# Kernel optimization log

Measured on AMD Instinct MI355X. Metric: run time of the kernel, lower is better.

The kernel has to match this reference:

```python
import jax, jax.numpy as jnp
import numpy as np

C = 8; E = 512; HEADS = 8; DH = E // HEADS; M = 256; PINV_ITERS = 6; KW = 33

def layer_norm(x, g, b):
    mu = x.mean(-1, keepdims=True)
    xm = x - mu
    v = (xm * xm).mean(-1, keepdims=True)
    return xm / jnp.sqrt(v + 1e-5) * g + b

def mp_pinv(x, iters=PINV_ITERS):
    # Moore-Penrose pseudoinverse via Newton-Schulz iterations (lucidrains nystrom-attention)
    I = jnp.eye(x.shape[-1], dtype=x.dtype)
    ax = jnp.abs(x)
    z = jnp.swapaxes(x, -1, -2) / (jnp.max(ax.sum(-2)) * jnp.max(ax.sum(-1)))
    for _ in range(iters):
        xz = x @ z
        z = 0.25 * z @ (13. * I - xz @ (15. * I - xz @ (7. * I - xz)))
    return z

def nystrom_attn(x, mask, Wqkv, Wout, bout, conv_w):
    b, n0, d = x.shape
    pad = (-n0) % M  # left-pad so seq divisible by num_landmarks
    x = jnp.pad(x, ((0, 0), (pad, 0), (0, 0)))
    mask = jnp.pad(mask, ((0, 0), (pad, 0)))
    n = n0 + pad
    qkv = (x @ Wqkv).reshape(b, n, 3, HEADS, DH).transpose(2, 0, 3, 1, 4)
    q, k, v = qkv[0], qkv[1], qkv[2]  # [b,h,n,dh]
    mf = mask[:, None, :, None].astype(x.dtype)
    q = q * mf * (DH ** -0.5); k = k * mf; v = v * mf
    l = n // M
    mls = mask.reshape(b, 1, M, l).sum(-1).astype(x.dtype)  # valid count per landmark segment
    div = mls[..., None] + 1e-8
    ql = q.reshape(b, HEADS, M, l, DH).sum(3) / div
    kl = k.reshape(b, HEADS, M, l, DH).sum(3) / div
    mland = mls > 0  # [b,1,M]
    neg = -jnp.finfo(x.dtype).max / 2
    sim1 = jnp.where(mask[:, None, :, None] & mland[..., None, :], jnp.einsum('bhid,bhjd->bhij', q, kl), neg)
    sim2 = jnp.where(mland[..., :, None] & mland[..., None, :], jnp.einsum('bhid,bhjd->bhij', ql, kl), neg)
    sim3 = jnp.where(mland[..., :, None] & mask[:, None, None, :], jnp.einsum('bhid,bhjd->bhij', ql, k), neg)
    a1 = jax.nn.softmax(sim1, -1); a2 = jax.nn.softmax(sim2, -1); a3 = jax.nn.softmax(sim3, -1)
    out = (a1 @ mp_pinv(a2)) @ (a3 @ v)
    # residual depthwise conv over sequence dim (residual=True in NystromAttention)
    out = out + jax.lax.conv_general_dilated(v, conv_w, (1, 1), ((KW // 2, KW // 2), (0, 0)),
                                             dimension_numbers=('NCHW', 'OIHW', 'NCHW'),
                                             feature_group_count=HEADS)
    out = out.transpose(0, 2, 1, 3).reshape(b, n, d) @ Wout + bout
    return out[:, pad:]

def _forward(h, W1, b1, cls_token, pmt_token, ln1_g, ln1_b, Wqkv1, Wout1, bout1, conv1,
             ln0_g, ln0_b, Wqkv0, Wout0, bout0, conv0, lnf_g, lnf_b, W3, b3):
    N = h.shape[0]
    h1 = jax.nn.relu(h @ W1 + b1)  # _fc1
    seq = jnp.concatenate([cls_token, pmt_token, h1], 0)[None]  # [1, 1+C+N, E]
    y = nystrom_attn(layer_norm(seq, ln1_g, ln1_b), jnp.ones((1, seq.shape[1]), bool),
                     Wqkv1, Wout1, bout1, conv1)
    x = seq + y  # layer1 (TransLayer_custom)
    pmt = x[:, 1:1 + C, :]   # new pmt tokens [1,C,E]
    toks = x[:, 1 + C:, :]   # [1,N,E]
    assn = jax.nn.softmax(jnp.einsum('bnd,bcd->bnc', toks, pmt), -1)
    idx = jnp.argmax(assn[0], -1)  # [N] cluster assignment
    # cluster dispatch: per-cluster [pmt_i; tokens-of-cluster-i] run of shared layer0, via masking
    xs = jnp.concatenate([pmt[0][:, None, :], jnp.broadcast_to(toks[0], (C, N, E))], 1)  # [C,1+N,E]
    masks = jnp.concatenate([jnp.ones((C, 1), bool), idx[None, :] == jnp.arange(C)[:, None]], 1)
    def trans0(xi, mi):
        xi = xi[None]
        return (xi + nystrom_attn(layer_norm(xi, ln0_g, ln0_b), mi[None], Wqkv0, Wout0, bout0, conv0))[0]
    out = jax.vmap(trans0)(xs, masks)  # [C,1+N,E]
    h_un = out[:, 1:, :][idx, jnp.arange(N)]  # each token from its own cluster's run
    order = jnp.argsort(idx)  # stable: groups tokens by cluster, preserving order (concat order)
    h_global = h_un[order]; idx_new = idx[order]
    hcat = jnp.concatenate([x[0, 0][None], h_global], 0)  # [1+N, E]
    hn = layer_norm(hcat, lnf_g, lnf_b)
    sums = jax.ops.segment_sum(hcat[1:], idx_new, num_segments=C)
    counts = jax.ops.segment_sum(jnp.ones((N,), h.dtype), idx_new, num_segments=C)
    merge = sums / jnp.maximum(counts, 1.)[:, None]  # CTM merge token per cluster
    ptc = jnp.linalg.norm(pmt[0] @ pmt[0].T - jnp.eye(C, dtype=h.dtype))
    tok_out = jnp.concatenate([hn[0][None], merge], 0).mean(0)
    logit = tok_out @ W3 + b3
    return logit, ptc

def setup_inputs() -> dict:
    key = jax.random.key(0)
    ks = jax.random.split(key, 16)
    N, IN_DIM, NC = 4096, 1024, 2
    s = 0.02
    q, _ = jnp.linalg.qr(jax.random.normal(ks[15], (E, C)))  # orthonormal pmt init
    return {
        'h': jax.random.normal(ks[0], (N, IN_DIM)),
        'W1': jax.random.normal(ks[1], (IN_DIM, E)) * s, 'b1': jnp.zeros((E,)),
        'cls_token': jax.random.normal(ks[2], (1, E)),
        'pmt_token': q.T,
        'ln1_g': jnp.ones((E,)), 'ln1_b': jnp.zeros((E,)),
        'Wqkv1': jax.random.normal(ks[3], (E, 3 * E)) * s,
        'Wout1': jax.random.normal(ks[4], (E, E)) * s, 'bout1': jnp.zeros((E,)),
        'conv1': jax.random.normal(ks[5], (HEADS, 1, KW, 1)) * s,
        'ln0_g': jnp.ones((E,)), 'ln0_b': jnp.zeros((E,)),
        'Wqkv0': jax.random.normal(ks[6], (E, 3 * E)) * s,
        'Wout0': jax.random.normal(ks[7], (E, E)) * s, 'bout0': jnp.zeros((E,)),
        'conv0': jax.random.normal(ks[8], (HEADS, 1, KW, 1)) * s,
        'lnf_g': jnp.ones((E,)), 'lnf_b': jnp.zeros((E,)),
        'W3': jax.random.normal(ks[9], (E, NC)) * s, 'b3': jnp.zeros((NC,)),
    }

def reference(h, W1, b1, cls_token, pmt_token, ln1_g, ln1_b, Wqkv1, Wout1, bout1, conv1,
              ln0_g, ln0_b, Wqkv0, Wout0, bout0, conv0, lnf_g, lnf_b, W3, b3):
    logit, ptc = _forward(h, W1, b1, cls_token, pmt_token, ln1_g, ln1_b, Wqkv1, Wout1, bout1, conv1,
                          ln0_g, ln0_b, Wqkv0, Wout0, bout0, conv0, lnf_g, lnf_b, W3, b3)
    return (logit[None], jax.nn.softmax(logit)[None], ptc)
```

## Files before the change

kernel.cpp:

```cpp
#include <hip/hip_runtime.h>

#define NEGV (-1.70141173e38f)

constexpr int E    = 512;
constexpr int NTOK = 4096;
constexpr int NPAD = 4352;
constexpr int PAD1 = 247;
constexpr int NSEQ = 4105;
constexpr int NG   = 5120;
constexpr int NTP  = 4104;

typedef __attribute__((ext_vector_type(8))) short short8;
typedef __attribute__((ext_vector_type(4))) float float4v;

__device__ inline float bf2f(ushort u){ return __uint_as_float(((unsigned)u)<<16); }
__device__ inline ushort f2bf(float f){
  unsigned u = __float_as_uint(f);
  unsigned r = (u + 0x7FFFu + ((u>>16)&1u)) >> 16;
  return (ushort)r;
}

template<int BT, bool BOUNDS>
__global__ __launch_bounds__(256) void k_mm(
    const ushort* __restrict__ A, const ushort* __restrict__ B,
    const float* __restrict__ bias, const float* __restrict__ resid,
    float* __restrict__ Cf, ushort* __restrict__ Cb,
    int M, int N, int K, int ksplit, int ldC,
    long sA, long sB, long sC,
    const int* __restrict__ colsel, const int* __restrict__ rowsel,
    int zmodA, int zmodB, const int* __restrict__ krange, int kshift,
    float alpha, float bdiag, int flags)
{
  const int z = blockIdx.z;
  const int batch = z / ksplit, ks = z - batch * ksplit;
  const int kslice = K / ksplit;
  int kbeg = ks * kslice, kend = kbeg + kslice;
  if (krange) { int ki = batch >> kshift; kbeg = krange[2*ki]; kend = krange[2*ki+1]; }
  long aoff;
  if (colsel) { int s = colsel[blockIdx.x]; if (s < 0) s = 0; aoff = (long)(s*8 + batch) * sA; }
  else aoff = (long)(zmodA ? (batch & (zmodA-1)) : batch) * sA;
  long boff;
  if (rowsel) { int s = rowsel[blockIdx.y]; if (s < 0) s = 0; boff = (long)(s*8 + batch) * sB; }
  else boff = (long)(zmodB ? (batch & (zmodB-1)) : batch) * sB;
  A += aoff; B += boff;
  const long coff = (long)z * sC;

  __shared__ __align__(16) ushort Al[4][128][8];
  __shared__ __align__(16) ushort Bl[4][128][8];

  const int tid  = threadIdx.x;
  const int lane = tid & 63, wid = tid >> 6;
  const int wr = wid >> 1, wc = wid & 1;
  const int l4 = lane >> 4, l15 = lane & 15;
  const int row0 = blockIdx.y * 128, col0 = blockIdx.x * 128;

  float4v acc[4][4];
#pragma unroll
  for (int i = 0; i < 4; ++i)
#pragma unroll
    for (int j = 0; j < 4; ++j) acc[i][j] = (float4v){0.f,0.f,0.f,0.f};

  for (int k0 = kbeg; k0 < kend; k0 += 32) {
    __syncthreads();
#pragma unroll
    for (int e = 0; e < 2; ++e) {
      int id = tid * 2 + e; int m = id >> 2, kb = id & 3;
      uint4 v = make_uint4(0u,0u,0u,0u);
      int gr = row0 + m;
      if (!BOUNDS || gr < M)
        v = *reinterpret_cast<const uint4*>(A + (long)gr * K + k0 + kb * 8);
      *reinterpret_cast<uint4*>(&Al[kb][m][0]) = v;
    }
    if (BT) {
#pragma unroll
      for (int e = 0; e < 2; ++e) {
        int id = tid * 2 + e; int n = id >> 2, kb = id & 3;
        uint4 v = make_uint4(0u,0u,0u,0u);
        int gc = col0 + n;
        if (!BOUNDS || gc < N)
          v = *reinterpret_cast<const uint4*>(B + (long)gc * K + k0 + kb * 8);
        *reinterpret_cast<uint4*>(&Bl[kb][n][0]) = v;
      }
    } else {
      int n = tid & 127, gc = col0 + n;
      bool inb = (!BOUNDS || gc < N);
#pragma unroll
      for (int e = 0; e < 2; ++e) {
        int kb = (tid >> 7) * 2 + e;
        ushort u[8];
#pragma unroll
        for (int j = 0; j < 8; ++j) {
          int gk = k0 + kb * 8 + j;
          ushort val = inb ? B[(long)gk * N + gc] : (ushort)0;
          if (flags & 4) {
            float f = bdiag * (gk == gc ? 1.f : 0.f) - bf2f(val);
            val = f2bf(f);
          }
          u[j] = val;
        }
        uint4 w;
        w.x = (unsigned)u[0] | ((unsigned)u[1] << 16);
        w.y = (unsigned)u[2] | ((unsigned)u[3] << 16);
        w.z = (unsigned)u[4] | ((unsigned)u[5] << 16);
        w.w = (unsigned)u[6] | ((unsigned)u[7] << 16);
        *reinterpret_cast<uint4*>(&Bl[kb][n][0]) = w;
      }
    }
    __syncthreads();
    short8 af[4], bg[4];
#pragma unroll
    for (int mi = 0; mi < 4; ++mi)
      af[mi] = *reinterpret_cast<const short8*>(&Al[l4][wr*64 + mi*16 + l15][0]);
#pragma unroll
    for (int ni = 0; ni < 4; ++ni)
      bg[ni] = *reinterpret_cast<const short8*>(&Bl[l4][wc*64 + ni*16 + l15][0]);
#pragma unroll
    for (int mi = 0; mi < 4; ++mi)
#pragma unroll
      for (int ni = 0; ni < 4; ++ni)
        acc[mi][ni] = __builtin_amdgcn_mfma_f32_16x16x32_bf16(af[mi], bg[ni], acc[mi][ni], 0, 0, 0);
  }
#pragma unroll
  for (int mi = 0; mi < 4; ++mi)
#pragma unroll
    for (int ni = 0; ni < 4; ++ni)
#pragma unroll
      for (int r = 0; r < 4; ++r) {
        int row = row0 + wr*64 + mi*16 + l4*4 + r;
        int col = col0 + wc*64 + ni*16 + l15;
        if (BOUNDS && (row >= M || col >= N)) continue;
        float v = alpha * acc[mi][ni][r];
        if (flags & 1) v += bias[col];
        if (flags & 2) v = fmaxf(v, 0.f);
        if (flags & 8) v += resid[(long)row * ldC + col];
        long off = coff + (long)row * ldC + col;
        if (flags & 16) Cb[off] = f2bf(v); else Cf[off] = v;
      }
}

static void mm(hipStream_t st, const void* A, const void* B, const float* bias, const float* resid,
               float* Cf, ushort* Cb, int M, int N, int K, int nb, int ksplit, int ldC,
               long sA, long sB, long sC,
               const int* colsel, const int* rowsel, int zmodA, int zmodB,
               const int* krange, int kshift,
               float alpha, float bdiag, int flags, bool bt, bool bounds)
{
  dim3 g((N + 127) / 128, (M + 127) / 128, nb * ksplit), b(256);
  const ushort* a = (const ushort*)A; const ushort* bb = (const ushort*)B;
  if (bt) {
    if (bounds) k_mm<1, true ><<<g, b, 0, st>>>(a, bb, bias, resid, Cf, Cb, M, N, K, ksplit, ldC, sA, sB, sC, colsel, rowsel, zmodA, zmodB, krange, kshift, alpha, bdiag, flags);
    else        k_mm<1, false><<<g, b, 0, st>>>(a, bb, bias, resid, Cf, Cb, M, N, K, ksplit, ldC, sA, sB, sC, colsel, rowsel, zmodA, zmodB, krange, kshift, alpha, bdiag, flags);
  } else {
    if (bounds) k_mm<0, true ><<<g, b, 0, st>>>(a, bb, bias, resid, Cf, Cb, M, N, K, ksplit, ldC, sA, sB, sC, colsel, rowsel, zmodA, zmodB, krange, kshift, alpha, bdiag, flags);
    else        k_mm<0, false><<<g, b, 0, st>>>(a, bb, bias, resid, Cf, Cb, M, N, K, ksplit, ldC, sA, sB, sC, colsel, rowsel, zmodA, zmodB, krange, kshift, alpha, bdiag, flags);
  }
}

static void pinv_iters(hipStream_t st, const ushort* PX, ushort* PZ, ushort* Y, ushort* T1, ushort* T2, int nb) {
  ushort* z = PZ; ushort* y = Y;
  for (int it = 0; it < 6; ++it) {
    mm(st, PX, z,  nullptr, nullptr, nullptr, y,  256,256,256, nb,1,256, 65536,65536,65536, nullptr,nullptr,0,0,nullptr,0, 1.f,   0.f, 16,    false, false);
    mm(st, y,  y,  nullptr, nullptr, nullptr, T1, 256,256,256, nb,1,256, 65536,65536,65536, nullptr,nullptr,0,0,nullptr,0, 1.f,   7.f, 16|4,  false, false);
    mm(st, y,  T1, nullptr, nullptr, nullptr, T2, 256,256,256, nb,1,256, 65536,65536,65536, nullptr,nullptr,0,0,nullptr,0, 1.f,  15.f, 16|4,  false, false);
    mm(st, z,  T2, nullptr, nullptr, nullptr, y,  256,256,256, nb,1,256, 65536,65536,65536, nullptr,nullptr,0,0,nullptr,0, 0.25f,13.f, 16|4,  false, false);
    ushort* tmp = z; z = y; y = tmp;
  }
}

__global__ void k_z0(const ushort* __restrict__ X, const float* __restrict__ sc, ushort* __restrict__ Z, int nb) {
  long t = (long)blockIdx.x * 256 + threadIdx.x;
  if (t >= (long)nb * 65536) return;
  int bt = (int)(t >> 16); int ij = (int)(t & 65535); int i = ij >> 8, j = ij & 255;
  Z[t] = f2bf(bf2f(X[((long)bt << 16) + j * 256 + i]) * sc[bt >> 3]);
}

__global__ __launch_bounds__(256) void k_colmax(const ushort* __restrict__ X, float* __restrict__ sc) {
  int cl = blockIdx.x, j = threadIdx.x;
  float cmax = 0.f;
  for (int h = 0; h < 8; ++h) {
    const ushort* mat = X + (long)(cl * 8 + h) * 65536;
    float cs = 0.f;
    for (int i = 0; i < 256; ++i) cs += bf2f(mat[i * 256 + j]);
    cmax = fmaxf(cmax, cs);
  }
  __shared__ float red[256];
  red[j] = cmax; __syncthreads();
  for (int o = 128; o > 0; o >>= 1) { if (j < o) red[j] = fmaxf(red[j], red[j + o]); __syncthreads(); }
  if (j == 0) sc[cl] = 1.f / red[0];
}

__global__ void k_prep0(const float* __restrict__ cls, const float* __restrict__ pmt, float* __restrict__ seq) {
  int i = blockIdx.x * 256 + threadIdx.x;
  if (i < 512) seq[i] = cls[i];
  else if (i < 4608) seq[i] = pmt[i - 512];
}
__global__ void k_cvt(const float* __restrict__ s, ushort* __restrict__ d, long n) {
  long i = (long)blockIdx.x * 256 + threadIdx.x;
  if (i < n) d[i] = f2bf(s[i]);
}
__global__ void k_tcvt_all(const float* __restrict__ W1, const float* __restrict__ Wq1,
                           const float* __restrict__ Wq0, const float* __restrict__ Wo1,
                           const float* __restrict__ Wo0,
                           ushort* __restrict__ W1t, ushort* __restrict__ Wq1t,
                           ushort* __restrict__ Wq0t, ushort* __restrict__ Wo1t,
                           ushort* __restrict__ Wo0t) {
  const float* W; ushort* Wt; int K, N;
  switch (blockIdx.z) {
    case 0:  W = W1;  Wt = W1t;  K = 1024; N = 512;  break;
    case 1:  W = Wq1; Wt = Wq1t; K = 512;  N = 1536; break;
    case 2:  W = Wq0; Wt = Wq0t; K = 512;  N = 1536; break;
    case 3:  W = Wo1; Wt = Wo1t; K = 512;  N = 512;  break;
    default: W = Wo0; Wt = Wo0t; K = 512;  N = 512;  break;
  }
  int nb_ = blockIdx.x * 32, kb = blockIdx.y * 32;
  if (nb_ >= N || kb >= K) return;
  __shared__ float tile[32][33];
  int tx = threadIdx.x, ty = threadIdx.y;
  for (int r = ty; r < 32; r += 8) tile[r][tx] = W[(long)(kb + r) * N + nb_ + tx];
  __syncthreads();
  for (int r = ty; r < 32; r += 8) Wt[(long)(nb_ + r) * K + kb + tx] = f2bf(tile[tx][r]);
}

__device__ __forceinline__ void ln_row(const float* __restrict__ xr, const float* __restrict__ g,
                                       const float* __restrict__ b, ushort* __restrict__ yr,
                                       float* red, int t) {
  float v0 = xr[t], v1 = xr[t + 256];
  red[t] = v0 + v1; __syncthreads();
  for (int o = 128; o > 0; o >>= 1) { if (t < o) red[t] += red[t + o]; __syncthreads(); }
  float mu = red[0] * (1.f / E); __syncthreads();
  float d0 = v0 - mu, d1 = v1 - mu;
  red[t] = d0 * d0 + d1 * d1; __syncthreads();
  for (int o = 128; o > 0; o >>= 1) { if (t < o) red[t] += red[t + o]; __syncthreads(); }
  float inv = 1.f / sqrtf(red[0] * (1.f / E) + 1e-5f);
  yr[t]       = f2bf(d0 * inv * g[t]       + b[t]);
  yr[t + 256] = f2bf(d1 * inv * g[t + 256] + b[t + 256]);
}

__global__ __launch_bounds__(256) void k_lnB(const float* __restrict__ x, const float* __restrict__ g,
                                             const float* __restrict__ b, ushort* __restrict__ y) {
  int row = blockIdx.x, t = threadIdx.x;
  ushort* yr = y + (long)row * E;
  if (row < PAD1) { yr[t] = 0; yr[t + 256] = 0; return; }
  __shared__ float red[256];
  ln_row(x + (long)(row - PAD1) * E, g, b, yr, red, t);
}
__global__ __launch_bounds__(256) void k_lnC(const float* __restrict__ seq, const float* __restrict__ g,
                                             const float* __restrict__ b, ushort* __restrict__ y) {
  int row = blockIdx.x, t = threadIdx.x;
  const float* xr = (row < 8) ? (seq + 512 + (long)row * E) : (seq + 9 * 512 + (long)(row - 8) * E);
  __shared__ float red[256];
  ln_row(xr, g, b, y + (long)row * E, red, t);
}

__global__ void k_buildQKVB(const float* __restrict__ qkv, ushort* __restrict__ Qb,
                            ushort* __restrict__ Kb, ushort* __restrict__ Vt) {
  int h = blockIdx.y, p0 = blockIdx.x * 64;
  int tx = threadIdx.x & 63, tg = threadIdx.x >> 6;
  __shared__ float tile[64][65];
  for (int r = tg; r < 64; r += 4) {
    long src = (long)(p0 + r) * 1536 + h * 64 + tx;
    long o = ((long)h * NPAD + p0 + r) * 64 + tx;
    Qb[o] = f2bf(qkv[src]);
    Kb[o] = f2bf(qkv[src + 512]);
    tile[r][tx] = qkv[src + 1024];
  }
  __syncthreads();
  for (int d = tg; d < 64; d += 4) Vt[((long)h * 64 + d) * NPAD + p0 + tx] = f2bf(tile[tx][d]);
}
__global__ void k_gatherQKV(const float* __restrict__ qkvall, const int* __restrict__ gtok,
                            ushort* __restrict__ Qg, ushort* __restrict__ Kg, ushort* __restrict__ Vgt) {
  int h = blockIdx.y, p0 = blockIdx.x * 64;
  int tx = threadIdx.x & 63, tg = threadIdx.x >> 6;
  __shared__ float tile[64][65];
  for (int r = tg; r < 64; r += 4) {
    int tk = gtok[p0 + r];
    int srcrow = tk >= 0 ? 8 + tk : (tk <= -2 ? (-2 - tk) : -1);
    float q = 0.f, k = 0.f, v = 0.f;
    if (srcrow >= 0) {
      long s = (long)srcrow * 1536 + h * 64 + tx;
      q = qkvall[s]; k = qkvall[s + 512]; v = qkvall[s + 1024];
    }
    long o = ((long)h * NG + p0 + r) * 64 + tx;
    Qg[o] = f2bf(q); Kg[o] = f2bf(k);
    tile[r][tx] = v;
  }
  __syncthreads();
  for (int d = tg; d < 64; d += 4) Vgt[((long)h * 64 + d) * NG + p0 + tx] = f2bf(tile[tx][d]);
}

__global__ void k_qlkl_B(const float* __restrict__ qkv, ushort* __restrict__ ql, ushort* __restrict__ kl,
                         float* __restrict__ mlandB) {
  int i = blockIdx.x, h = blockIdx.y, d = threadIdx.x;
  float sq = 0.f, sk = 0.f; int cnt = 0;
  for (int j = 0; j < 17; ++j) {
    int p = i * 17 + j;
    if (p >= PAD1) {
      sq += qkv[(long)p * 1536 + h * 64 + d];
      sk += qkv[(long)p * 1536 + 512 + h * 64 + d];
      cnt++;
    }
  }
  float dv = (float)cnt + 1e-8f;
  ql[((long)h * 256 + i) * 64 + d] = f2bf(sq * 0.125f / dv);
  kl[((long)h * 256 + i) * 64 + d] = f2bf(sk / dv);
  if (h == 0 && d == 0) mlandB[i] = cnt > 0 ? 1.f : 0.f;
}

__global__ void k_qlkl_C(const float* __restrict__ qkvall, const int* __restrict__ idx,
                         ushort* __restrict__ qlc, ushort* __restrict__ klc,
                         float* __restrict__ mland_c) {
  int i = blockIdx.x, bt = blockIdx.y;
  int c = bt >> 3, h = bt & 7, d = threadIdx.x;
  float sq = 0.f, sk = 0.f; int cnt = 0;
  for (int j = 0; j < 17; ++j) {
    int p = i * 17 + j;
    int srcrow = -1;
    if (p == 255) srcrow = c;
    else if (p >= 256 && idx[p - 256] == c) srcrow = 8 + (p - 256);
    if (srcrow >= 0) {
      const float* src = qkvall + (long)srcrow * 1536 + h * 64;
      sq += src[d]; sk += src[512 + d];
      cnt++;
    }
  }
  float dv = (float)cnt + 1e-8f;
  qlc[((long)bt * 256 + i) * 64 + d] = f2bf(sq * 0.125f / dv);
  klc[((long)bt * 256 + i) * 64 + d] = f2bf(sk / dv);
  if (h == 0 && d == 0) mland_c[c * 256 + i] = cnt > 0 ? 1.f : 0.f;
}

__global__ __launch_bounds__(256) void k_a2soft(const float* __restrict__ S2, const float* __restrict__ mland,
                                                ushort* __restrict__ X) {
  int i = blockIdx.x, bt = blockIdx.y, j = threadIdx.x;
  int cl = bt >> 3;
  const float* Sr = S2 + ((long)bt * 256 + i) * 256;
  __shared__ float red[256];
  float landi = mland[cl * 256 + i];
  float out;
  if (landi > 0.f) {
    bool valid = mland[cl * 256 + j] > 0.f;
    float sv = valid ? Sr[j] : NEGV;
    red[j] = sv; __syncthreads();
    for (int o = 128; o > 0; o >>= 1) { if (j < o) red[j] = fmaxf(red[j], red[j + o]); __syncthreads(); }
    float mx = red[0]; __syncthreads();
    float e = valid ? expf(sv - mx) : 0.f;
    red[j] = e; __syncthreads();
    for (int o = 128; o > 0; o >>= 1) { if (j < o) red[j] += red[j + o]; __syncthreads(); }
    out = e / red[0];
  } else {
    out = 1.f / 256.f;
  }
  X[((long)bt * 256 + i) * 256 + j] = f2bf(out);
}

__global__ __launch_bounds__(256) void k_smaxB_av(const float* __restrict__ S, ushort* __restrict__ P,
                                                  const float* __restrict__ mland) {
  int i = blockIdx.x, h = blockIdx.y, t = threadIdx.x;
  const float* Sr = S + ((long)h * 256 + i) * NPAD;
  ushort* Pr = P + ((long)h * 256 + i) * NPAD;
  __shared__ float sv[NPAD];
  __shared__ float red[256];
  if (mland[i] > 0.f) {
    float lmax = NEGV;
    for (int j = t; j < NPAD; j += 256) {
      float s = Sr[j];
      sv[j] = s;
      if (j >= PAD1) lmax = fmaxf(lmax, s);
    }
    red[t] = lmax; __syncthreads();
    for (int o = 128; o > 0; o >>= 1) { if (t < o) red[t] = fmaxf(red[t], red[t + o]); __syncthreads(); }
    float mx = red[0]; __syncthreads();
    float lsum = 0.f;
    for (int j = t; j < NPAD; j += 256) {
      float e = (j >= PAD1) ? expf(sv[j] - mx) : 0.f;
      sv[j] = e; lsum += e;
    }
    red[t] = lsum; __syncthreads();
    for (int o = 128; o > 0; o >>= 1) { if (t < o) red[t] += red[t + o]; __syncthreads(); }
    float inv = 1.f / red[0];
    for (int j = t; j < NPAD; j += 256) Pr[j] = f2bf(sv[j] * inv);
  } else {
    const float u = 1.f / 4352.f;
    for (int j = t; j < NPAD; j += 256) Pr[j] = f2bf(j >= PAD1 ? u : 0.f);
  }
}

__global__ __launch_bounds__(256) void k_smaxseg(const float* __restrict__ S3, ushort* __restrict__ P3,
                                                 const float* __restrict__ mlandC, const int* __restrict__ gclu,
                                                 const int* __restrict__ segb) {
  int i = blockIdx.x, bt = blockIdx.y, t = threadIdx.x;
  int c = bt >> 3, h = bt & 7;
  const float* Sr = S3 + ((long)h * 256 + i) * NG;
  ushort* Pr = P3 + ((long)h * 256 + i) * NG;
  int jb = segb[c], je = segb[c + 1];
  __shared__ float sv[4352];
  __shared__ float red[256];
  if (mlandC[c * 256 + i] > 0.f) {
    float lmax = NEGV;
    for (int j = jb + t; j < je; j += 256) {
      float s = Sr[j];
      sv[j - jb] = s;
      if (gclu[j] == c) lmax = fmaxf(lmax, s);
    }
    red[t] = lmax; __syncthreads();
    for (int o = 128; o > 0; o >>= 1) { if (t < o) red[t] = fmaxf(red[t], red[t + o]); __syncthreads(); }
    float mx = red[0]; __syncthreads();
    float lsum = 0.f;
    for (int j = jb + t; j < je; j += 256) {
      float e = (gclu[j] == c) ? expf(sv[j - jb] - mx) : 0.f;
      sv[j - jb] = e; lsum += e;
    }
    red[t] = lsum; __syncthreads();
    for (int o = 128; o > 0; o >>= 1) { if (t < o) red[t] += red[t + o]; __syncthreads(); }
    float inv = 1.f / red[0];
    for (int j = jb + t; j < je; j += 256) Pr[j] = f2bf(sv[j - jb] * inv);
  } else {
    const float u = 1.f / 4352.f;
    for (int j = jb + t; j < je; j += 256) Pr[j] = f2bf(gclu[j] == c ? u : 0.f);
  }
}

template<int MODE>
__global__ __launch_bounds__(256) void k_smax256(const float* __restrict__ S, ushort* __restrict__ P,
                                                 const float* __restrict__ mland, const int* __restrict__ gtok,
                                                 const int* __restrict__ gclu, int rows) {
  int row = blockIdx.x, h = blockIdx.y, j = threadIdx.x;
  const float* Sr = S + ((long)h * rows + row) * 256;
  ushort* Pr = P + ((long)h * rows + row) * 256;
  int c = 0;
  if (MODE == 1) {
    int tk = gtok[row];
    if (tk < 0) { Pr[j] = 0; return; }
    c = gclu[row];
  }
  bool mem = (MODE == 1) ? (mland[c * 256 + j] > 0.f) : (mland[j] > 0.f);
  __shared__ float red[256];
  float s = mem ? Sr[j] : NEGV;
  red[j] = s; __syncthreads();
  for (int o = 128; o > 0; o >>= 1) { if (j < o) red[j] = fmaxf(red[j], red[j + o]); __syncthreads(); }
  float mx = red[0]; __syncthreads();
  float e = mem ? expf(s - mx) : 0.f;
  red[j] = e; __syncthreads();
  for (int o = 128; o > 0; o >>= 1) { if (j < o) red[j] += red[j + o]; __syncthreads(); }
  Pr[j] = f2bf(e / red[0]);
}

__global__ void k_avredB(const float* __restrict__ sl, ushort* __restrict__ avb, int ks) {
  int i = blockIdx.x, h = blockIdx.y, d = threadIdx.x;
  float s = 0.f;
  for (int k = 0; k < ks; ++k) s += sl[(((long)h * ks + k) * 256 + i) * 64 + d];
  avb[((long)h * 256 + i) * 64 + d] = f2bf(s);
}

__global__ void k_conv_B(const float* __restrict__ qkv, const float* __restrict__ w,
                         const float* __restrict__ preout, ushort* __restrict__ lnb) {
  int r = blockIdx.x, t = threadIdx.x;
  int h = t >> 6;
  int prow = PAD1 + r;
  float acc = preout[(long)prow * E + t];
  for (int tt = 0; tt < 33; ++tt) {
    int p = prow + tt - 16;
    if (p < NPAD) acc += qkv[(long)p * 1536 + 1024 + t] * w[h * 33 + tt];
  }
  lnb[(long)r * E + t] = f2bf(acc);
}

__global__ void k_idxptc(const float* __restrict__ x, int* __restrict__ idx, float* __restrict__ ptc_out) {
  int t = threadIdx.x;
  __shared__ float red[64];
  if (blockIdx.x == NTOK) {
    int a = t >> 3, b = t & 7;
    const float* pmt = x + E;
    float s = 0.f;
    for (int d = 0; d < E; ++d) s += pmt[(long)a * E + d] * pmt[(long)b * E + d];
    s -= (a == b) ? 1.f : 0.f;
    red[t] = s * s; __syncthreads();
    for (int o = 32; o > 0; o >>= 1) { if (t < o) red[t] += red[t + o]; __syncthreads(); }
    if (t == 0) *ptc_out = sqrtf(red[0]);
    return;
  }
  int n = blockIdx.x;
  const float* tok = x + (long)(9 + n) * E;
  const float* pmt = x + E;
  int c = t >> 3, part = t & 7;
  float s = 0.f;
  for (int d = part * 64; d < part * 64 + 64; ++d) s += tok[d] * pmt[(long)c * E + d];
  red[t] = s; __syncthreads();
  if (t < 8) {
    float dot = 0.f;
    for (int p = 0; p < 8; ++p) dot += red[t * 8 + p];
    red[t] = dot;
  }
  __syncthreads();
  if (t == 0) {
    int best = 0; float bv = red[0];
    for (int c2 = 1; c2 < 8; ++c2) if (red[c2] > bv) { bv = red[c2]; best = c2; }
    idx[n] = best;
  }
}

__global__ __launch_bounds__(256) void k_gprep(const int* __restrict__ idx, int* __restrict__ gtok,
                                               int* __restrict__ gclu, int* __restrict__ gpos,
                                               int* __restrict__ segb, int* __restrict__ krange,
                                               int* __restrict__ blkclu) {
  __shared__ int hist[8][16];
  __shared__ int boff[8][16];
  __shared__ int segs[9];
  __shared__ int sidx[256];
  int t = threadIdx.x;
  if (t < 128) ((int*)hist)[t] = 0;
  __syncthreads();
  for (int b = 0; b < 16; ++b) atomicAdd(&hist[idx[b * 256 + t]][b], 1);
  __syncthreads();
  if (t == 0) {
    int s = 0;
    for (int c = 0; c < 8; ++c) {
      segs[c] = s;
      int run = s + 1, tot = 1;
      for (int b = 0; b < 16; ++b) { boff[c][b] = run; run += hist[c][b]; tot += hist[c][b]; }
      krange[2 * c] = s;
      krange[2 * c + 1] = s + ((tot + 31) & ~31);
      s += (tot + 127) & ~127;
    }
    segs[8] = s;
    for (int c = 0; c <= 8; ++c) segb[c] = segs[c];
  }
  __syncthreads();
  for (int g = t; g < NG; g += 256) { gtok[g] = -1; gclu[g] = -1; }
  __syncthreads();
  if (t < 8) { gtok[segs[t]] = -2 - t; gclu[segs[t]] = t; }
  for (int b = t; b < NG / 128; b += 256) {
    int cl = -1;
    for (int c = 0; c < 8; ++c) if (b * 128 >= segs[c] && b * 128 < segs[c + 1]) cl = c;
    blkclu[b] = cl;
  }
  for (int b = 0; b < 16; ++b) {
    int n = b * 256 + t;
    int c = idx[n];
    sidx[t] = c;
    __syncthreads();
    int rank = 0;
    for (int m = 0; m < t; ++m) rank += (sidx[m] == c);
    int pos = boff[c][b] + rank;
    gtok[pos] = n; gclu[pos] = c; gpos[n] = pos;
    __syncthreads();
  }
}

__global__ void k_outC(const float* __restrict__ OUTg, const int* __restrict__ gpos,
                       const int* __restrict__ idx, const float* __restrict__ qkvall,
                       const float* __restrict__ w, ushort* __restrict__ lnb) {
  int n = blockIdx.x, t = threadIdx.x;
  int h = t >> 6;
  int c = idx[n];
  float acc = OUTg[(long)gpos[n] * 512 + t];
  for (int tt = 0; tt < 33; ++tt) {
    int m = n + tt - 16;
    float vv = 0.f;
    if (m == -1) vv = qkvall[(long)c * 1536 + 1024 + t];
    else if (m >= 0 && m < NTOK && idx[m] == c) vv = qkvall[(long)(8 + m) * 1536 + 1024 + t];
    acc += vv * w[h * 33 + tt];
  }
  lnb[(long)n * E + t] = f2bf(acc);
}

__global__ void k_seg_part(const float* __restrict__ hun, const int* __restrict__ idx,
                           float* __restrict__ part, float* __restrict__ pcnt) {
  int c = blockIdx.x, sl = blockIdx.y, d = threadIdx.x;
  float s = 0.f; int cnt = 0;
  for (int n = sl * 256; n < sl * 256 + 256; ++n) {
    if (idx[n] == c) { s += hun[(long)n * E + d]; if (d == 0) cnt++; }
  }
  part[(long)(c * 16 + sl) * E + d] = s;
  if (d == 0) pcnt[c * 16 + sl] = (float)cnt;
}

__global__ void k_final(const float* __restrict__ x0, const float* __restrict__ g, const float* __restrict__ b,
                        const float* __restrict__ part, const float* __restrict__ pcnt,
                        const float* __restrict__ ptc, const float* __restrict__ W3, const float* __restrict__ b3,
                        float* __restrict__ out) {
  int t = threadIdx.x;
  __shared__ float red[512];
  float xv = x0[t];
  red[t] = xv; __syncthreads();
  for (int o = 256; o > 0; o >>= 1) { if (t < o) red[t] += red[t + o]; __syncthreads(); }
  float mu = red[0] * (1.f / 512.f); __syncthreads();
  float d0 = xv - mu;
  red[t] = d0 * d0; __syncthreads();
  for (int o = 256; o > 0; o >>= 1) { if (t < o) red[t] += red[t + o]; __syncthreads(); }
  float inv = 1.f / sqrtf(red[0] * (1.f / 512.f) + 1e-5f);
  __syncthreads();
  float acc = d0 * inv * g[t] + b[t];
  for (int c = 0; c < 8; ++c) {
    float s = 0.f, cnt = 0.f;
    for (int sl = 0; sl < 16; ++sl) { s += part[(long)(c * 16 + sl) * E + t]; cnt += pcnt[c * 16 + sl]; }
    acc += s / fmaxf(cnt, 1.f);
  }
  float tk = acc * (1.f / 9.f);
  red[t] = tk * W3[t * 2 + 0]; __syncthreads();
  for (int o = 256; o > 0; o >>= 1) { if (t < o) red[t] += red[t + o]; __syncthreads(); }
  float l0 = red[0] + b3[0]; __syncthreads();
  red[t] = tk * W3[t * 2 + 1]; __syncthreads();
  for (int o = 256; o > 0; o >>= 1) { if (t < o) red[t] += red[t + o]; __syncthreads(); }
  float l1 = red[0] + b3[1];
  if (t == 0) {
    out[0] = l0; out[1] = l1;
    float mx = fmaxf(l0, l1);
    float e0 = expf(l0 - mx), e1 = expf(l1 - mx), s = e0 + e1;
    out[2] = e0 / s; out[3] = e1 / s;
    out[4] = *ptc;
  }
}

extern "C" void kernel_launch(void* const* d_in, const int* in_sizes, int n_in,
                              void* d_out, int out_size, void* d_ws, size_t ws_size,
                              hipStream_t stream) {
  const float* h_in  = (const float*)d_in[0];
  const float* W1    = (const float*)d_in[1];
  const float* b1    = (const float*)d_in[2];
  const float* cls   = (const float*)d_in[3];
  const float* pmt_t = (const float*)d_in[4];
  const float* ln1_g = (const float*)d_in[5];
  const float* ln1_b = (const float*)d_in[6];
  const float* Wqkv1 = (const float*)d_in[7];
  const float* Wout1 = (const float*)d_in[8];
  const float* bout1 = (const float*)d_in[9];
  const float* conv1 = (const float*)d_in[10];
  const float* ln0_g = (const float*)d_in[11];
  const float* ln0_b = (const float*)d_in[12];
  const float* Wqkv0 = (const float*)d_in[13];
  const float* Wout0 = (const float*)d_in[14];
  const float* bout0 = (const float*)d_in[15];
  const float* conv0 = (const float*)d_in[16];
  const float* lnf_g = (const float*)d_in[17];
  const float* lnf_b = (const float*)d_in[18];
  const float* W3    = (const float*)d_in[19];
  const float* b3    = (const float*)d_in[20];

  char* base = (char*)d_ws;
  size_t off = 0;
  auto alloc = [&](size_t b) -> void* {
    off = (off + 255) & ~(size_t)255;
    void* p = base + off; off += b; return p;
  };
  float*  SEQ    = (float*) alloc((size_t)NSEQ * E * 4);
  float*  QKV    = (float*) alloc((size_t)NPAD * 1536 * 4);
  ushort* W1t    = (ushort*)alloc((size_t)512 * 1024 * 2);
  ushort* Wq1t   = (ushort*)alloc((size_t)1536 * 512 * 2);
  ushort* Wq0t   = (ushort*)alloc((size_t)1536 * 512 * 2);
  ushort* Wo1t   = (ushort*)alloc((size_t)512 * 512 * 2);
  ushort* Wo0t   = (ushort*)alloc((size_t)512 * 512 * 2);
  ushort* LNb    = (ushort*)alloc((size_t)NPAD * E * 2);
  ushort* QbU    = (ushort*)alloc((size_t)8 * NG * 64 * 2);
  ushort* KbU    = (ushort*)alloc((size_t)8 * NG * 64 * 2);
  ushort* VtU    = (ushort*)alloc((size_t)8 * NG * 64 * 2);
  char*   U1     = (char*)  alloc((size_t)8 * 256 * NG * 4);
  char*   U2     = (char*)  alloc((size_t)8 * 256 * NG * 2);
  ushort* PXb    = (ushort*)alloc((size_t)64 * 65536 * 2);
  ushort* PZa    = (ushort*)alloc((size_t)64 * 65536 * 2);
  ushort* qlbB   = (ushort*)alloc((size_t)8 * 16384 * 2);
  ushort* klbB   = (ushort*)alloc((size_t)8 * 16384 * 2);
  ushort* qlcb   = (ushort*)alloc((size_t)64 * 16384 * 2);
  ushort* klcb   = (ushort*)alloc((size_t)64 * 16384 * 2);
  float*  avsl   = (float*) alloc((size_t)8 * 8 * 16384 * 4);
  ushort* avb    = (ushort*)alloc((size_t)64 * 16384 * 2);
  ushort* Wcb    = (ushort*)alloc((size_t)64 * 16384 * 2);
  float*  PREOUT = (float*) alloc((size_t)NPAD * E * 4);
  float*  mlandB = (float*) alloc(256 * 4);
  float*  mlandC = (float*) alloc(8 * 256 * 4);
  int*    idx    = (int*)   alloc(NTOK * 4);
  int*    gtok   = (int*)   alloc(NG * 4);
  int*    gclu   = (int*)   alloc(NG * 4);
  int*    gpos   = (int*)   alloc(NTOK * 4);
  int*    segb   = (int*)   alloc(9 * 4);
  int*    krange = (int*)   alloc(16 * 4);
  int*    blkclu = (int*)   alloc((NG / 128) * 4);
  float*  ptc    = (float*) alloc(256);
  float*  sc     = (float*) alloc(256);
  float*  part   = (float*) alloc((size_t)8 * 16 * 512 * 4);
  float*  pcnt   = (float*) alloc(8 * 16 * 4);

  ushort* hb   = (ushort*)U1;
  float*  Sbuf = (float*)U1;
  ushort* Ybuf = (ushort*)U1;
  ushort* T1c  = (ushort*)(U1 + (size_t)64 * 65536 * 2);
  ushort* T2c  = (ushort*)(U1 + (size_t)2 * 64 * 65536 * 2);
  float*  OUTg = (float*)U1;
  ushort* Pbuf = (ushort*)U2;

  k_tcvt_all<<<dim3(48, 32, 5), dim3(32, 8), 0, stream>>>(W1, Wqkv1, Wqkv0, Wout1, Wout0,
                                                          W1t, Wq1t, Wq0t, Wo1t, Wo0t);
  k_prep0<<<dim3(18), dim3(256), 0, stream>>>(cls, pmt_t, SEQ);
  k_cvt<<<dim3(16384), dim3(256), 0, stream>>>(h_in, hb, (long)4096 * 1024);
  mm(stream, hb, W1t, b1, nullptr, SEQ + 9 * 512, nullptr, 4096, 512, 1024, 1, 1, 512,
     0, 0, 0, nullptr, nullptr, 0, 0, nullptr, 0, 1.f, 0.f, 1 | 2, true, false);

  k_lnB<<<dim3(NPAD), dim3(256), 0, stream>>>(SEQ, ln1_g, ln1_b, LNb);
  mm(stream, LNb, Wq1t, nullptr, nullptr, QKV, nullptr, NPAD, 1536, 512, 1, 1, 1536,
     0, 0, 0, nullptr, nullptr, 0, 0, nullptr, 0, 1.f, 0.f, 0, true, false);
  k_buildQKVB<<<dim3(NPAD / 64, 8), dim3(256), 0, stream>>>(QKV, QbU, KbU, VtU);
  k_qlkl_B<<<dim3(256, 8), dim3(64), 0, stream>>>(QKV, qlbB, klbB, mlandB);
  mm(stream, qlbB, klbB, nullptr, nullptr, Sbuf, nullptr, 256, 256, 64, 8, 1, 256,
     16384, 16384, 65536, nullptr, nullptr, 0, 0, nullptr, 0, 1.f, 0.f, 0, true, false);
  k_a2soft<<<dim3(256, 8), dim3(256), 0, stream>>>(Sbuf, mlandB, PXb);
  k_colmax<<<dim3(1), dim3(256), 0, stream>>>(PXb, sc);
  k_z0<<<dim3((8 * 65536) / 256), dim3(256), 0, stream>>>(PXb, sc, PZa, 8);
  pinv_iters(stream, PXb, PZa, Ybuf, T1c, T2c, 8);
  mm(stream, qlbB, KbU, nullptr, nullptr, Sbuf, nullptr, 256, NPAD, 64, 8, 1, NPAD,
     16384, (long)NPAD * 64, (long)256 * NPAD, nullptr, nullptr, 0, 0, nullptr, 0, 1.f, 0.f, 0, true, false);
  k_smaxB_av<<<dim3(256, 8), dim3(256), 0, stream>>>(Sbuf, Pbuf, mlandB);
  mm(stream, Pbuf, VtU, nullptr, nullptr, avsl, nullptr, 256, 64, NPAD, 8, 8, 64,
     (long)256 * NPAD, (long)64 * NPAD, 16384, nullptr, nullptr, 0, 0, nullptr, 0, 1.f, 0.f, 0, true, true);
  k_avredB<<<dim3(256, 8), dim3(64), 0, stream>>>(avsl, avb, 8);
  mm(stream, PZa, avb, nullptr, nullptr, nullptr, Wcb, 256, 64, 256, 8, 1, 64,
     65536, 16384, 16384, nullptr, nullptr, 0, 0, nullptr, 0, 1.f, 0.f, 16, false, true);
  mm(stream, QbU + PAD1 * 64, klbB, nullptr, nullptr, Sbuf, nullptr, NSEQ, 256, 64, 8, 1, 256,
     (long)NPAD * 64, 16384, (long)NSEQ * 256, nullptr, nullptr, 0, 0, nullptr, 0, 0.125f, 0.f, 0, true, true);
  k_smax256<0><<<dim3(NSEQ, 8), dim3(256), 0, stream>>>(Sbuf, Pbuf, mlandB, nullptr, nullptr, NSEQ);
  mm(stream, Pbuf, Wcb, nullptr, nullptr, PREOUT + (long)PAD1 * 512, nullptr, NSEQ, 64, 256, 8, 1, 512,
     (long)NSEQ * 256, 16384, 64, nullptr, nullptr, 0, 0, nullptr, 0, 1.f, 0.f, 0, false, true);
  k_conv_B<<<dim3(NSEQ), dim3(512), 0, stream>>>(QKV, conv1, PREOUT, LNb);
  mm(stream, LNb, Wo1t, bout1, SEQ, SEQ, nullptr, NSEQ, 512, 512, 1, 1, 512,
     0, 0, 0, nullptr, nullptr, 0, 0, nullptr, 0, 1.f, 0.f, 1 | 8, true, true);

  k_idxptc<<<dim3(NTOK + 1), dim3(64), 0, stream>>>(SEQ, idx, ptc);
  k_gprep<<<dim3(1), dim3(256), 0, stream>>>(idx, gtok, gclu, gpos, segb, krange, blkclu);
  k_lnC<<<dim3(NTP), dim3(256), 0, stream>>>(SEQ, ln0_g, ln0_b, LNb);
  mm(stream, LNb, Wq0t, nullptr, nullptr, QKV, nullptr, NTP, 1536, 512, 1, 1, 1536,
     0, 0, 0, nullptr, nullptr, 0, 0, nullptr, 0, 1.f, 0.f, 0, true, true);
  k_qlkl_C<<<dim3(256, 64), dim3(64), 0, stream>>>(QKV, idx, qlcb, klcb, mlandC);
  k_gatherQKV<<<dim3(NG / 64, 8), dim3(256), 0, stream>>>(QKV, gtok, QbU, KbU, VtU);
  mm(stream, qlcb, klcb, nullptr, nullptr, Sbuf, nullptr, 256, 256, 64, 64, 1, 256,
     16384, 16384, 65536, nullptr, nullptr, 0, 0, nullptr, 0, 1.f, 0.f, 0, true, false);
  k_a2soft<<<dim3(256, 64), dim3(256), 0, stream>>>(Sbuf, mlandC, PXb);
  k_colmax<<<dim3(8), dim3(256), 0, stream>>>(PXb, sc);
  k_z0<<<dim3((64 * 65536) / 256), dim3(256), 0, stream>>>(PXb, sc, PZa, 64);
  pinv_iters(stream, PXb, PZa, Ybuf, T1c, T2c, 64);
  mm(stream, qlcb, KbU, nullptr, nullptr, Sbuf, nullptr, 256, NG, 64, 8, 1, NG,
     16384, (long)NG * 64, (long)256 * NG, blkclu, nullptr, 0, 0, nullptr, 0, 1.f, 0.f, 0, true, false);
  k_smaxseg<<<dim3(256, 64), dim3(256), 0, stream>>>(Sbuf, Pbuf, mlandC, gclu, segb);
  mm(stream, Pbuf, VtU, nullptr, nullptr, nullptr, avb, 256, 64, NG, 64, 1, 64,
     (long)256 * NG, (long)64 * NG, 16384, nullptr, nullptr, 8, 8, krange, 3, 1.f, 0.f, 16, true, true);
  mm(stream, PZa, avb, nullptr, nullptr, nullptr, Wcb, 256, 64, 256, 64, 1, 64,
     65536, 16384, 16384, nullptr, nullptr, 0, 0, nullptr, 0, 1.f, 0.f, 16, false, true);
  mm(stream, QbU, klcb, nullptr, nullptr, Sbuf, nullptr, NG, 256, 64, 8, 1, 256,
     (long)NG * 64, 16384, (long)NG * 256, nullptr, blkclu, 0, 0, nullptr, 0, 0.125f, 0.f, 0, true, false);
  k_smax256<1><<<dim3(NG, 8), dim3(256), 0, stream>>>(Sbuf, Pbuf, mlandC, gtok, gclu, NG);
  mm(stream, Pbuf, Wcb, nullptr, nullptr, OUTg, nullptr, NG, 64, 256, 8, 1, 512,
     (long)NG * 256, 16384, 64, nullptr, blkclu, 0, 0, nullptr, 0, 1.f, 0.f, 0, false, true);
  k_outC<<<dim3(NTOK), dim3(512), 0, stream>>>(OUTg, gpos, idx, QKV, conv0, LNb);
  mm(stream, LNb, Wo0t, bout0, SEQ + 9 * 512, PREOUT, nullptr, NTOK, 512, 512, 1, 1, 512,
     0, 0, 0, nullptr, nullptr, 0, 0, nullptr, 0, 1.f, 0.f, 1 | 8, true, false);

  k_seg_part<<<dim3(8, 16), dim3(512), 0, stream>>>(PREOUT, idx, part, pcnt);
  k_final<<<dim3(1), dim3(512), 0, stream>>>(SEQ, lnf_g, lnf_b, part, pcnt, ptc, W3, b3,
                                             (float*)d_out);
}
```

Measured before the change: 2.612 ms.

## Fuse pseudoinverse iterations into one persistent kernel with grid barriers

Replaces the colmax, z0 init and 24 separate GEMM launches of the Newton-Schulz pseudoinverse with a single persistent kernel. The kernel uses atomic grid-wide barriers and writes each result plus its transpose, so B operands load contiguously without the strided per-element gather. Separately, the token grouping prep is rewritten to rank tokens with wave ballots and popcounts instead of an O(n) per-thread scan. This removes launch overhead and uncoalesced B loads, but adds spin-barrier cost, doubled output writes, and a co-residency assumption for 256 blocks.

After: 2.993 ms. +14.6%, slower.

```diff
diff --git a/kernel.cpp b/kernel.cpp
--- a/kernel.cpp
+++ b/kernel.cpp
@@ -18,6 +18,14 @@
   unsigned u = __float_as_uint(f);
   unsigned r = (u + 0x7FFFu + ((u>>16)&1u)) >> 16;
   return (ushort)r;
+}
+__device__ inline uint4 packu4(const ushort* u) {
+  uint4 w;
+  w.x = (unsigned)u[0] | ((unsigned)u[1] << 16);
+  w.y = (unsigned)u[2] | ((unsigned)u[3] << 16);
+  w.z = (unsigned)u[4] | ((unsigned)u[5] << 16);
+  w.w = (unsigned)u[6] | ((unsigned)u[7] << 16);
+  return w;
 }
 
 template<int BT, bool BOUNDS>
@@ -98,12 +106,7 @@
           }
           u[j] = val;
         }
-        uint4 w;
-        w.x = (unsigned)u[0] | ((unsigned)u[1] << 16);
-        w.y = (unsigned)u[2] | ((unsigned)u[3] << 16);
-        w.z = (unsigned)u[4] | ((unsigned)u[5] << 16);
-        w.w = (unsigned)u[6] | ((unsigned)u[7] << 16);
-        *reinterpret_cast<uint4*>(&Bl[kb][n][0]) = w;
+        *reinterpret_cast<uint4*>(&Bl[kb][n][0]) = packu4(u);
       }
     }
     __syncthreads();
@@ -156,37 +159,181 @@
   }
 }
 
-static void pinv_iters(hipStream_t st, const ushort* PX, ushort* PZ, ushort* Y, ushort* T1, ushort* T2, int nb) {
-  ushort* z = PZ; ushort* y = Y;
+__global__ __launch_bounds__(256, 1) void k_pinv(
+    const ushort* __restrict__ X,
+    ushort* __restrict__ ZA, ushort* __restrict__ ZAt,
+    ushort* __restrict__ ZB, ushort* __restrict__ ZBt,
+    ushort* __restrict__ Y,  ushort* __restrict__ Yt,
+    ushort* __restrict__ T1, ushort* __restrict__ T1t,
+    ushort* __restrict__ T2, ushort* __restrict__ T2t,
+    float* __restrict__ sc, int nb, int* __restrict__ bars)
+{
+  __shared__ __align__(16) ushort SH[8448];
+  ushort* AlF = SH;
+  ushort* BlF = SH + 4096;
+  const int tid = threadIdx.x;
+  const int nblk = gridDim.x;
+  int bi = 0;
+
+  auto BAR = [&]() {
+    __syncthreads();
+    if (tid == 0) {
+      __threadfence();
+      atomicAdd(&bars[bi], 1);
+      while (atomicAdd(&bars[bi], 0) < nblk) __builtin_amdgcn_s_sleep(2);
+    }
+    ++bi;
+    __syncthreads();
+    __threadfence();
+  };
+
+  {
+    int ncl = nb >> 3;
+    if ((int)blockIdx.x < ncl) {
+      float* red = (float*)SH;
+      int cl = blockIdx.x;
+      float cmax = 0.f;
+      for (int h = 0; h < 8; ++h) {
+        const ushort* mat = X + (long)(cl * 8 + h) * 65536;
+        float cs = 0.f;
+        for (int i = 0; i < 256; ++i) cs += bf2f(mat[i * 256 + tid]);
+        cmax = fmaxf(cmax, cs);
+      }
+      red[tid] = cmax; __syncthreads();
+      for (int o = 128; o > 0; o >>= 1) { if (tid < o) red[tid] = fmaxf(red[tid], red[tid+o]); __syncthreads(); }
+      if (tid == 0) sc[cl] = 1.f / red[0];
+    }
+    BAR();
+  }
+
+  const int ntile = nb * 4;
+
+  {
+    ushort (*lds2)[264] = (ushort(*)[264])SH;
+    for (int tile = blockIdx.x; tile < ntile; tile += nblk) {
+      int bt = tile >> 2, q = tile & 3;
+      int row0 = (q >> 1) * 128, col0 = (q & 1) * 128;
+      float scale = sc[bt >> 3];
+      const ushort* Xb = X + (long)bt * 65536;
+      ushort* Z0  = ZA  + (long)bt * 65536;
+      ushort* Z0t = ZAt + (long)bt * 65536;
+#pragma unroll
+      for (int e = 0; e < 8; ++e) {
+        int id = tid + e * 256;
+        int r = id >> 4, ch = (id & 15) * 8;
+        const ushort* src = Xb + (long)(row0 + r) * 256 + col0 + ch;
+        ushort u[8];
+#pragma unroll
+        for (int j = 0; j < 8; ++j) u[j] = f2bf(bf2f(src[j]) * scale);
+        *reinterpret_cast<uint4*>(Z0t + (long)(row0 + r) * 256 + col0 + ch) = packu4(u);
+      }
+      for (int s = 0; s < 4; ++s) {
+        __syncthreads();
+#pragma unroll
+        for (int e = 0; e < 2; ++e) {
+          int id = tid * 2 + e;
+          int sr = id >> 4, ch = (id & 15) * 8;
+          *reinterpret_cast<uint4*>(&lds2[sr][ch]) =
+            *reinterpret_cast<const uint4*>(Xb + (long)(col0 + s * 32 + sr) * 256 + row0 + ch);
+        }
+        __syncthreads();
+#pragma unroll
+        for (int e = 0; e < 2; ++e) {
+          int id = tid * 2 + e;
+          int orow = id >> 2, oseg = (id & 3) * 8;
+          ushort u[8];
+#pragma unroll
+          for (int j = 0; j < 8; ++j) u[j] = f2bf(bf2f(lds2[oseg + j][orow]) * scale);
+          *reinterpret_cast<uint4*>(Z0 + (long)(row0 + orow) * 256 + col0 + s * 32 + oseg) = packu4(u);
+        }
+      }
+      __syncthreads();
+    }
+    BAR();
+  }
+
+  const int lane = tid & 63, wid = tid >> 6;
+  const int wr = wid >> 1, wc = wid & 1;
+  const int l4 = lane >> 4, l15 = lane & 15;
+
+  auto GEMM = [&](const ushort* A, const ushort* Bt, ushort* C, ushort* Ct,
+                  float alpha, float bdiag, bool diag) {
+    for (int tile = blockIdx.x; tile < ntile; tile += nblk) {
+      int bt = tile >> 2, q = tile & 3;
+      int row0 = (q >> 1) * 128, col0 = (q & 1) * 128;
+      const ushort* Ab = A + (long)bt * 65536;
+      const ushort* Bb = Bt + (long)bt * 65536;
+      float4v acc[4][4];
+#pragma unroll
+      for (int i = 0; i < 4; ++i)
+#pragma unroll
+        for (int j = 0; j < 4; ++j) acc[i][j] = (float4v){0.f,0.f,0.f,0.f};
+      for (int k0 = 0; k0 < 256; k0 += 32) {
+        __syncthreads();
+#pragma unroll
+        for (int e = 0; e < 2; ++e) {
+          int id = tid * 2 + e; int m = id >> 2, kb = id & 3;
+          *reinterpret_cast<uint4*>(AlF + kb * 1024 + m * 8) =
+            *reinterpret_cast<const uint4*>(Ab + (long)(row0 + m) * 256 + k0 + kb * 8);
+        }
+#pragma unroll
+        for (int e = 0; e < 2; ++e) {
+          int id = tid * 2 + e; int n = id >> 2, kb = id & 3;
+          uint4 v = *reinterpret_cast<const uint4*>(Bb + (long)(col0 + n) * 256 + k0 + kb * 8);
+          if (diag) {
+            const ushort* up = reinterpret_cast<const ushort*>(&v);
+            ushort u2[8];
+#pragma unroll
+            for (int j = 0; j < 8; ++j) {
+              int gk = k0 + kb * 8 + j;
+              u2[j] = f2bf(bdiag * (gk == (col0 + n) ? 1.f : 0.f) - bf2f(up[j]));
+            }
+            v = packu4(u2);
+          }
+          *reinterpret_cast<uint4*>(BlF + kb * 1024 + n * 8) = v;
+        }
+        __syncthreads();
+        short8 af[4], bg[4];
+#pragma unroll
+        for (int mi = 0; mi < 4; ++mi)
+          af[mi] = *reinterpret_cast<const short8*>(AlF + l4 * 1024 + (wr * 64 + mi * 16 + l15) * 8);
+#pragma unroll
+        for (int ni = 0; ni < 4; ++ni)
+          bg[ni] = *reinterpret_cast<const short8*>(BlF + l4 * 1024 + (wc * 64 + ni * 16 + l15) * 8);
+#pragma unroll
+        for (int mi = 0; mi < 4; ++mi)
+#pragma unroll
+          for (int ni = 0; ni < 4; ++ni)
+            acc[mi][ni] = __builtin_amdgcn_mfma_f32_16x16x32_bf16(af[mi], bg[ni], acc[mi][ni], 0, 0, 0);
+      }
+      long cb = (long)bt * 65536;
+#pragma unroll
+      for (int mi = 0; mi < 4; ++mi)
+#pragma unroll
+        for (int ni = 0; ni < 4; ++ni)
+#pragma unroll
+          for (int r = 0; r < 4; ++r) {
+            int row = row0 + wr * 64 + mi * 16 + l4 * 4 + r;
+            int col = col0 + wc * 64 + ni * 16 + l15;
+            ushort val = f2bf(alpha * acc[mi][ni][r]);
+            C[cb + (long)row * 256 + col] = val;
+            Ct[cb + (long)col * 256 + row] = val;
+          }
+      __syncthreads();
+    }
+  };
+
   for (int it = 0; it < 6; ++it) {
-    mm(st, PX, z,  nullptr, nullptr, nullptr, y,  256,256,256, nb,1,256, 65536,65536,65536, nullptr,nullptr,0,0,nullptr,0, 1.f,   0.f, 16,    false, false);
-    mm(st, y,  y,  nullptr, nullptr, nullptr, T1, 256,256,256, nb,1,256, 65536,65536,65536, nullptr,nullptr,0,0,nullptr,0, 1.f,   7.f, 16|4,  false, false);
-    mm(st, y,  T1, nullptr, nullptr, nullptr, T2, 256,256,256, nb,1,256, 65536,65536,65536, nullptr,nullptr,0,0,nullptr,0, 1.f,  15.f, 16|4,  false, false);
-    mm(st, z,  T2, nullptr, nullptr, nullptr, y,  256,256,256, nb,1,256, 65536,65536,65536, nullptr,nullptr,0,0,nullptr,0, 0.25f,13.f, 16|4,  false, false);
-    ushort* tmp = z; z = y; y = tmp;
-  }
-}
-
-__global__ void k_z0(const ushort* __restrict__ X, const float* __restrict__ sc, ushort* __restrict__ Z, int nb) {
-  long t = (long)blockIdx.x * 256 + threadIdx.x;
-  if (t >= (long)nb * 65536) return;
-  int bt = (int)(t >> 16); int ij = (int)(t & 65535); int i = ij >> 8, j = ij & 255;
-  Z[t] = f2bf(bf2f(X[((long)bt << 16) + j * 256 + i]) * sc[bt >> 3]);
-}
-
-__global__ __launch_bounds__(256) void k_colmax(const ushort* __restrict__ X, float* __restrict__ sc) {
-  int cl = blockIdx.x, j = threadIdx.x;
-  float cmax = 0.f;
-  for (int h = 0; h < 8; ++h) {
-    const ushort* mat = X + (long)(cl * 8 + h) * 65536;
-    float cs = 0.f;
-    for (int i = 0; i < 256; ++i) cs += bf2f(mat[i * 256 + j]);
-    cmax = fmaxf(cmax, cs);
-  }
-  __shared__ float red[256];
-  red[j] = cmax; __syncthreads();
-  for (int o = 128; o > 0; o >>= 1) { if (j < o) red[j] = fmaxf(red[j], red[j + o]); __syncthreads(); }
-  if (j == 0) sc[cl] = 1.f / red[0];
+    ushort* Zc  = (it & 1) ? ZB  : ZA;
+    ushort* Zct = (it & 1) ? ZBt : ZAt;
+    ushort* Zn  = (it & 1) ? ZA  : ZB;
+    ushort* Znt = (it & 1) ? ZAt : ZBt;
+    GEMM(X,  Zct, Y,  Yt,  1.f,    0.f, false); BAR();
+    GEMM(Y,  Yt,  T1, T1t, 1.f,    7.f, true);  BAR();
+    GEMM(Y,  T1t, T2, T2t, 1.f,   15.f, true);  BAR();
+    GEMM(Zc, T2t, Zn, Znt, 0.25f, 13.f, true);
+    if (it < 5) BAR();
+  }
 }
 
 __global__ void k_prep0(const float* __restrict__ cls, const float* __restrict__ pmt, float* __restrict__ seq) {
@@ -503,24 +650,34 @@
                                                int* __restrict__ gclu, int* __restrict__ gpos,
                                                int* __restrict__ segb, int* __restrict__ krange,
                                                int* __restrict__ blkclu) {
-  __shared__ int hist[8][16];
-  __shared__ int boff[8][16];
+  __shared__ int wcnt[4][8];
+  __shared__ int tot[8];
+  __shared__ int base[8];
   __shared__ int segs[9];
-  __shared__ int sidx[256];
-  int t = threadIdx.x;
-  if (t < 128) ((int*)hist)[t] = 0;
+  int t = threadIdx.x, lane = t & 63, w = t >> 6;
+  unsigned long long ltmask = (1ull << lane) - 1ull;
+  if (t < 8) tot[t] = 0;
   __syncthreads();
-  for (int b = 0; b < 16; ++b) atomicAdd(&hist[idx[b * 256 + t]][b], 1);
-  __syncthreads();
+  int myc[16];
+  for (int b = 0; b < 16; ++b) {
+    myc[b] = idx[b * 256 + t];
+    for (int cc = 0; cc < 8; ++cc) {
+      unsigned long long m = __ballot(myc[b] == cc);
+      if (lane == 0) wcnt[w][cc] = __popcll(m);
+    }
+    __syncthreads();
+    if (t < 8) tot[t] += wcnt[0][t] + wcnt[1][t] + wcnt[2][t] + wcnt[3][t];
+    __syncthreads();
+  }
   if (t == 0) {
     int s = 0;
     for (int c = 0; c < 8; ++c) {
       segs[c] = s;
-      int run = s + 1, tot = 1;
-      for (int b = 0; b < 16; ++b) { boff[c][b] = run; run += hist[c][b]; tot += hist[c][b]; }
+      base[c] = s + 1;
+      int tt2 = 1 + tot[c];
       krange[2 * c] = s;
-      krange[2 * c + 1] = s + ((tot + 31) & ~31);
-      s += (tot + 127) & ~127;
+      krange[2 * c + 1] = s + ((tt2 + 31) & ~31);
+      s += (tt2 + 127) & ~127;
     }
     segs[8] = s;
     for (int c = 0; c <= 8; ++c) segb[c] = segs[c];
@@ -535,14 +692,20 @@
     blkclu[b] = cl;
   }
   for (int b = 0; b < 16; ++b) {
+    int c = myc[b];
+    int rankw = 0;
+    for (int cc = 0; cc < 8; ++cc) {
+      unsigned long long m = __ballot(c == cc);
+      if (c == cc) rankw = __popcll(m & ltmask);
+      if (lane == 0) wcnt[w][cc] = __popcll(m);
+    }
+    __syncthreads();
+    int off = base[c] + rankw;
+    for (int w2 = 0; w2 < w; ++w2) off += wcnt[w2][c];
     int n = b * 256 + t;
-    int c = idx[n];
-    sidx[t] = c;
+    gtok[off] = n; gclu[off] = c; gpos[n] = off;
     __syncthreads();
-    int rank = 0;
-    for (int m = 0; m < t; ++m) rank += (sidx[m] == c);
-    int pos = boff[c][b] + rank;
-    gtok[pos] = n; gclu[pos] = c; gpos[n] = pos;
+    if (t < 8) base[t] += wcnt[0][t] + wcnt[1][t] + wcnt[2][t] + wcnt[3][t];
     __syncthreads();
   }
 }
@@ -658,6 +821,7 @@
   char*   U2     = (char*)  alloc((size_t)8 * 256 * NG * 2);
   ushort* PXb    = (ushort*)alloc((size_t)64 * 65536 * 2);
   ushort* PZa    = (ushort*)alloc((size_t)64 * 65536 * 2);
+  ushort* PZat   = (ushort*)alloc((size_t)64 * 65536 * 2);
   ushort* qlbB   = (ushort*)alloc((size_t)8 * 16384 * 2);
   ushort* klbB   = (ushort*)alloc((size_t)8 * 16384 * 2);
   ushort* qlcb   = (ushort*)alloc((size_t)64 * 16384 * 2);
@@ -677,16 +841,24 @@
   int*    blkclu = (int*)   alloc((NG / 128) * 4);
   float*  ptc    = (float*) alloc(256);
   float*  sc     = (float*) alloc(256);
+  int*    bars   = (int*)   alloc(64 * 4);
   float*  part   = (float*) alloc((size_t)8 * 16 * 512 * 4);
   float*  pcnt   = (float*) alloc(8 * 16 * 4);
 
   ushort* hb   = (ushort*)U1;
   float*  Sbuf = (float*)U1;
-  ushort* Ybuf = (ushort*)U1;
-  ushort* T1c  = (ushort*)(U1 + (size_t)64 * 65536 * 2);
-  ushort* T2c  = (ushort*)(U1 + (size_t)2 * 64 * 65536 * 2);
+  ushort* Yp   = (ushort*)U1;
+  ushort* Ytp  = (ushort*)(U1 + 1L * 8388608);
+  ushort* T1p  = (ushort*)(U1 + 2L * 8388608);
+  ushort* T1tp = (ushort*)(U1 + 3L * 8388608);
+  ushort* T2p  = (ushort*)(U1 + 4L * 8388608);
   float*  OUTg = (float*)U1;
   ushort* Pbuf = (ushort*)U2;
+  ushort* ZBp  = (ushort*)U2;
+  ushort* ZBtp = (ushort*)U2 + 4194304;
+  ushort* T2tp = (ushort*)avsl;
+
+  hipMemsetAsync(bars, 0, 64 * sizeof(int), stream);
 
   k_tcvt_all<<<dim3(48, 32, 5), dim3(32, 8), 0, stream>>>(W1, Wqkv1, Wqkv0, Wout1, Wout0,
                                                           W1t, Wq1t, Wq0t, Wo1t, Wo0t);
@@ -703,9 +875,8 @@
   mm(stream, qlbB, klbB, nullptr, nullptr, Sbuf, nullptr, 256, 256, 64, 8, 1, 256,
      16384, 16384, 65536, nullptr, nullptr, 0, 0, nullptr, 0, 1.f, 0.f, 0, true, false);
   k_a2soft<<<dim3(256, 8), dim3(256), 0, stream>>>(Sbuf, mlandB, PXb);
-  k_colmax<<<dim3(1), dim3(256), 0, stream>>>(PXb, sc);
-  k_z0<<<dim3((8 * 65536) / 256), dim3(256), 0, stream>>>(PXb, sc, PZa, 8);
-  pinv_iters(stream, PXb, PZa, Ybuf, T1c, T2c, 8);
+  k_pinv<<<dim3(256), dim3(256), 0, stream>>>(PXb, PZa, PZat, ZBp, ZBtp, Yp, Ytp, T1p, T1tp, T2p, T2tp,
+                                              sc, 8, bars);
   mm(stream, qlbB, KbU, nullptr, nullptr, Sbuf, nullptr, 256, NPAD, 64, 8, 1, NPAD,
      16384, (long)NPAD * 64, (long)256 * NPAD, nullptr, nullptr, 0, 0, nullptr, 0, 1.f, 0.f, 0, true, false);
   k_smaxB_av<<<dim3(256, 8), dim3(256), 0, stream>>>(Sbuf, Pbuf, mlandB);
@@ -733,9 +904,8 @@
   mm(stream, qlcb, klcb, nullptr, nullptr, Sbuf, nullptr, 256, 256, 64, 64, 1, 256,
      16384, 16384, 65536, nullptr, nullptr, 0, 0, nullptr, 0, 1.f, 0.f, 0, true, false);
   k_a2soft<<<dim3(256, 64), dim3(256), 0, stream>>>(Sbuf, mlandC, PXb);
-  k_colmax<<<dim3(8), dim3(256), 0, stream>>>(PXb, sc);
-  k_z0<<<dim3((64 * 65536) / 256), dim3(256), 0, stream>>>(PXb, sc, PZa, 64);
-  pinv_iters(stream, PXb, PZa, Ybuf, T1c, T2c, 64);
+  k_pinv<<<dim3(256), dim3(256), 0, stream>>>(PXb, PZa, PZat, ZBp, ZBtp, Yp, Ytp, T1p, T1tp, T2p, T2tp,
+                                              sc, 64, bars + 32);
   mm(stream, qlcb, KbU, nullptr, nullptr, Sbuf, nullptr, 256, NG, 64, 8, 1, NG,
      16384, (long)NG * 64, (long)256 * NG, blkclu, nullptr, 0, 0, nullptr, 0, 1.f, 0.f, 0, true, false);
   k_smaxseg<<<dim3(256, 64), dim3(256), 0, stream>>>(Sbuf, Pbuf, mlandC, gclu, segb);
```
